# Kernel tuning notes

Measured on AMD Instinct MI355X. Metric: run time of the kernel, lower is better.

## Reference

```python
import jax, jax.numpy as jnp
import numpy as np

D_MODEL = 1024
N_HEAD = 16
DEPTH = D_MODEL // N_HEAD
NEG = -10000.0


def setup_inputs() -> dict:
    key = jax.random.key(0)
    ks = jax.random.split(key, 10)
    B, N = 4, 2048
    s = 1.0 / np.sqrt(D_MODEL)
    inp = {
        "input": jax.random.normal(ks[0], (B, N, D_MODEL), dtype=jnp.float32),
        "mask": jnp.tril(jnp.ones((N, N), dtype=bool)),  # causal; True = attend
        "Wq": jax.random.normal(ks[1], (D_MODEL, D_MODEL), dtype=jnp.float32) * s,
        "bq": jnp.zeros((D_MODEL,), dtype=jnp.float32),
        "Wk": jax.random.normal(ks[2], (D_MODEL, D_MODEL), dtype=jnp.float32) * s,
        "bk": jnp.zeros((D_MODEL,), dtype=jnp.float32),
        "Wv": jax.random.normal(ks[3], (D_MODEL, D_MODEL), dtype=jnp.float32) * s,
        "bv": jnp.zeros((D_MODEL,), dtype=jnp.float32),
        "Wo": jax.random.normal(ks[4], (D_MODEL, D_MODEL), dtype=jnp.float32) * s,
        "bo": jnp.zeros((D_MODEL,), dtype=jnp.float32),
    }
    return inp


def reference(input, mask, Wq, bq, Wk, bk, Wv, bv, Wo, bo):
    b, n, _ = input.shape
    # torch Linear: x @ W.T + b  (dropout is identity in eval)
    q = (input @ Wq.T + bq).reshape(b, n, N_HEAD, DEPTH)
    k = (input @ Wk.T + bk).reshape(b, n, N_HEAD, DEPTH)
    v = (input @ Wv.T + bv).reshape(b, n, N_HEAD, DEPTH)
    # per-head scale is sqrt(depth) (ScaledDotProductAttention built with d_model=depth)
    scale = jnp.sqrt(jnp.asarray(DEPTH, dtype=input.dtype))
    scores = jnp.einsum("bnhd,bmhd->bhnm", q, k) / scale
    scores = jnp.where(mask, scores, NEG)
    attn = jax.nn.softmax(scores, axis=-1)
    out = jnp.einsum("bhnm,bmhd->bnhd", attn, v).reshape(b, n, D_MODEL)
    return out @ Wo.T + bo
```

## Files before the change

kernel.cpp:

```cpp
#include <hip/hip_runtime.h>
#include <hip/hip_bf16.h>
#include <stdint.h>

#define D_MODEL 1024
#define N_HEAD  16
#define DEPTH   64
#define BATCH   4
#define SEQ     2048
#define ROWS    (BATCH*SEQ)
#define LOG2E   1.4426950408889634f
#define QSCALE  0.18033688292839513f

typedef unsigned short u16;
typedef __attribute__((ext_vector_type(8))) short short8;
typedef __attribute__((ext_vector_type(4))) float f32x4;

__device__ inline u16 f2bf(float f) {
  union { float f; unsigned u; } v; v.f = f;
  unsigned r = v.u + 0x7FFFu + ((v.u >> 16) & 1u);
  return (u16)(r >> 16);
}

__device__ inline unsigned cvt_pk_bf16(float lo, float hi) {
  unsigned w;
  asm("v_cvt_pk_bf16_f32 %0, %1, %2" : "=v"(w) : "v"(lo), "v"(hi));
  return w;
}

__device__ inline void gll16(const void* g, void* l) {
  __builtin_amdgcn_global_load_lds(
      (const __attribute__((address_space(1))) void*)g,
      (__attribute__((address_space(3))) void*)l, 16, 0, 0);
}

__global__ __launch_bounds__(256) void cvt_all(
    const float4* __restrict__ X,  const float4* __restrict__ Wq,
    const float4* __restrict__ Wk, const float4* __restrict__ Wv,
    const float4* __restrict__ Wo,
    u16* __restrict__ Xb, u16* __restrict__ Wqkvb, u16* __restrict__ Wob)
{
  const int b = blockIdx.x;
  const float4* src; u16* dst; int lb;
  if      (b < 8192)  { src = X;  dst = Xb;                        lb = b; }
  else if (b < 9216)  { src = Wq; dst = Wqkvb;                     lb = b - 8192; }
  else if (b < 10240) { src = Wk; dst = Wqkvb + D_MODEL*D_MODEL;   lb = b - 9216; }
  else if (b < 11264) { src = Wv; dst = Wqkvb + 2*D_MODEL*D_MODEL; lb = b - 10240; }
  else                { src = Wo; dst = Wob;                       lb = b - 11264; }
  const int i = lb*256 + threadIdx.x;
  float4 v = src[i];
  ushort4 o;
  o.x = f2bf(v.x); o.y = f2bf(v.y); o.z = f2bf(v.z); o.w = f2bf(v.w);
  *(ushort4*)(dst + 4*(size_t)i) = o;
}

__global__ __launch_bounds__(256) void gemm_qkv(
    const u16* __restrict__ A, const u16* __restrict__ Bm,
    const float* __restrict__ bq, const float* __restrict__ bk,
    const float* __restrict__ bvp,
    u16* __restrict__ Qo, u16* __restrict__ Ko, u16* __restrict__ Vo)
{
  constexpr int K = D_MODEL, BK = 64;
  __shared__ __align__(16) u16 As[128*BK];
  __shared__ __align__(16) u16 Bs[128*BK];
  const int tid = threadIdx.x;
  const int wave = tid >> 6, lane = tid & 63;
  const int g = lane >> 4, c = lane & 15;
  const int m0 = blockIdx.x * 128, n0 = blockIdx.y * 128;
  const int wr = (wave >> 1) * 64, wc = (wave & 1) * 64;
  f32x4 acc[4][4] = {};

  int aRow[4], aCol[4];
#pragma unroll
  for (int cc = 0; cc < 4; ++cc) {
    int L = (wave*4 + cc)*1024 + lane*16;
    int U = L ^ (((L >> 7) & 7) << 4);
    aRow[cc] = U >> 7;
    aCol[cc] = (U & 127) >> 1;
  }

  for (int k0 = 0; k0 < K; k0 += BK) {
#pragma unroll
    for (int cc = 0; cc < 4; ++cc) {
      int chunk = wave*4 + cc;
      gll16(A  + (size_t)(m0 + aRow[cc])*K + k0 + aCol[cc], (char*)As + chunk*1024);
      gll16(Bm + (size_t)(n0 + aRow[cc])*K + k0 + aCol[cc], (char*)Bs + chunk*1024);
    }
    __syncthreads();
#pragma unroll
    for (int ks = 0; ks < 2; ++ks) {
      short8 af[4], bf[4];
#pragma unroll
      for (int rb = 0; rb < 4; ++rb) {
        int row = wr + rb*16 + c;
        int addr = (row*128 + ks*64 + g*16) ^ ((row & 7) << 4);
        af[rb] = *(const short8*)((const char*)As + addr);
      }
#pragma unroll
      for (int cb = 0; cb < 4; ++cb) {
        int row = wc + cb*16 + c;
        int addr = (row*128 + ks*64 + g*16) ^ ((row & 7) << 4);
        bf[cb] = *(const short8*)((const char*)Bs + addr);
      }
#pragma unroll
      for (int rb = 0; rb < 4; ++rb)
#pragma unroll
        for (int cb = 0; cb < 4; ++cb)
          acc[rb][cb] = __builtin_amdgcn_mfma_f32_16x16x32_bf16(af[rb], bf[cb], acc[rb][cb], 0, 0, 0);
    }
    __syncthreads();
  }

  const int mode = n0 >> 10;
  const float* bias = (mode == 0) ? bq : (mode == 1) ? bk : bvp;

#pragma unroll
  for (int rb = 0; rb < 4; ++rb) {
#pragma unroll
    for (int cb = 0; cb < 4; ++cb) {
      int colg = n0 + wc + cb*16 + c;
      int cl = colg & 1023;
      int h = cl >> 6, d = cl & 63;
      float bv = bias[cl];
      if (mode == 2) {
        int rg = m0 + wr + rb*16 + g*4;
        int b = rg >> 11, n = rg & 2047;
        ushort4 o;
        o.x = f2bf(acc[rb][cb][0] + bv);
        o.y = f2bf(acc[rb][cb][1] + bv);
        o.z = f2bf(acc[rb][cb][2] + bv);
        o.w = f2bf(acc[rb][cb][3] + bv);
        *(ushort4*)&Vo[(((size_t)(b*N_HEAD + h))*DEPTH + d)*SEQ + n] = o;
      } else {
        u16* dst = (mode == 0) ? Qo : Ko;
        float sc = (mode == 0) ? QSCALE : 1.0f;
#pragma unroll
        for (int r = 0; r < 4; ++r) {
          int rowg = m0 + wr + rb*16 + g*4 + r;
          int b = rowg >> 11, n = rowg & 2047;
          dst[(((size_t)(b*N_HEAD + h))*SEQ + n)*DEPTH + d] = f2bf((acc[rb][cb][r] + bv) * sc);
        }
      }
    }
  }
}

__global__ __launch_bounds__(256) void gemm_out(
    const u16* __restrict__ A, const u16* __restrict__ Bm,
    const float* __restrict__ bias, float* __restrict__ Cout,
    int M, int N, int K)
{
  constexpr int BK = 64;
  __shared__ __align__(16) u16 As[128*BK];
  __shared__ __align__(16) u16 Bs[128*BK];
  const int tid = threadIdx.x;
  const int wave = tid >> 6, lane = tid & 63;
  const int g = lane >> 4, c = lane & 15;
  const int m0 = blockIdx.x * 128, n0 = blockIdx.y * 128;
  const int wr = (wave >> 1) * 64, wc = (wave & 1) * 64;
  f32x4 acc[4][4] = {};

  int aRow[4], aCol[4];
#pragma unroll
  for (int cc = 0; cc < 4; ++cc) {
    int L = (wave*4 + cc)*1024 + lane*16;
    int U = L ^ (((L >> 7) & 7) << 4);
    aRow[cc] = U >> 7;
    aCol[cc] = (U & 127) >> 1;
  }

  for (int k0 = 0; k0 < K; k0 += BK) {
#pragma unroll
    for (int cc = 0; cc < 4; ++cc) {
      int chunk = wave*4 + cc;
      gll16(A  + (size_t)(m0 + aRow[cc])*K + k0 + aCol[cc], (char*)As + chunk*1024);
      gll16(Bm + (size_t)(n0 + aRow[cc])*K + k0 + aCol[cc], (char*)Bs + chunk*1024);
    }
    __syncthreads();
#pragma unroll
    for (int ks = 0; ks < 2; ++ks) {
      short8 af[4], bf[4];
#pragma unroll
      for (int rb = 0; rb < 4; ++rb) {
        int row = wr + rb*16 + c;
        int addr = (row*128 + ks*64 + g*16) ^ ((row & 7) << 4);
        af[rb] = *(const short8*)((const char*)As + addr);
      }
#pragma unroll
      for (int cb = 0; cb < 4; ++cb) {
        int row = wc + cb*16 + c;
        int addr = (row*128 + ks*64 + g*16) ^ ((row & 7) << 4);
        bf[cb] = *(const short8*)((const char*)Bs + addr);
      }
#pragma unroll
      for (int rb = 0; rb < 4; ++rb)
#pragma unroll
        for (int cb = 0; cb < 4; ++cb)
          acc[rb][cb] = __builtin_amdgcn_mfma_f32_16x16x32_bf16(af[rb], bf[cb], acc[rb][cb], 0, 0, 0);
    }
    __syncthreads();
  }

#pragma unroll
  for (int rb = 0; rb < 4; ++rb) {
#pragma unroll
    for (int cb = 0; cb < 4; ++cb) {
      int colg = n0 + wc + cb*16 + c;
      float bv = bias[colg];
#pragma unroll
      for (int r = 0; r < 4; ++r) {
        int rowg = m0 + wr + rb*16 + g*4 + r;
        Cout[(size_t)rowg * N + colg] = acc[rb][cb][r] + bv;
      }
    }
  }
}

__global__ __launch_bounds__(256) void flash(
    const u16* __restrict__ Q, const u16* __restrict__ K,
    const u16* __restrict__ VT, u16* __restrict__ O)
{
  __shared__ __align__(16) u16 Ks[2][64*64];
  __shared__ __align__(16) u16 Vs[2][64*64];
  const int tid = threadIdx.x, wave = tid >> 6, lane = tid & 63;
  const int g = lane >> 4, c = lane & 15;
  const int bid = blockIdx.x;
  const int qt = 31 - (bid >> 6);
  const int bh = bid & 63, b = bh >> 4, h = bh & 15;
  const int q0 = qt * 64;
  const int qg = q0 + wave*16 + c;
  const u16* Qh = Q  + (size_t)bh * SEQ * DEPTH;
  const u16* Kh = K  + (size_t)bh * SEQ * DEPTH;
  const u16* Vh = VT + (size_t)bh * DEPTH * SEQ;

  short8 qf[2];
#pragma unroll
  for (int ks = 0; ks < 2; ++ks)
    qf[ks] = *(const short8*)(Qh + (size_t)qg*DEPTH + ks*32 + g*8);

  f32x4 o[4] = {};
  float m_r = -3.0e38f, l_r = 0.0f;

  const int src1 = (c + (((2*g)  & 3) << 4)) << 2;
  const int src2 = (c + (((2*g+1)& 3) << 4)) << 2;
  const bool hi = (g >> 1) & 1;

  int sRow[2], sCol[2];
#pragma unroll
  for (int cc = 0; cc < 2; ++cc) {
    int L = (wave*2 + cc)*1024 + lane*16;
    int U = L ^ (((L >> 7) & 7) << 4);
    sRow[cc] = U >> 7; sCol[cc] = (U & 127) >> 1;
  }

  auto stage = [&](int t, int bsel) {
    const int kv0 = t * 64;
#pragma unroll
    for (int cc = 0; cc < 2; ++cc) {
      int chunk = wave*2 + cc;
      gll16(Kh + (size_t)(kv0 + sRow[cc])*DEPTH + sCol[cc], (char*)Ks[bsel] + chunk*1024);
      gll16(Vh + (size_t)sRow[cc]*SEQ + kv0 + sCol[cc],     (char*)Vs[bsel] + chunk*1024);
    }
  };

  const int ntiles = qt + 1;
  stage(0, 0);
  __syncthreads();
  int cur = 0;

  for (int t = 0; t < ntiles; ++t) {
    if (t + 1 < ntiles) stage(t + 1, cur ^ 1);
    const int kv0 = t * 64;
    const char* Kc = (const char*)Ks[cur];
    const char* Vc = (const char*)Vs[cur];

    f32x4 s[4] = {};
    __builtin_amdgcn_s_setprio(1);
#pragma unroll
    for (int ks = 0; ks < 2; ++ks)
#pragma unroll
      for (int cb = 0; cb < 4; ++cb) {
        int row = cb*16 + c;
        int addr = (row*128 + ks*64 + g*16) ^ ((row & 7) << 4);
        short8 kf = *(const short8*)(Kc + addr);
        s[cb] = __builtin_amdgcn_mfma_f32_16x16x32_bf16(kf, qf[ks], s[cb], 0, 0, 0);
      }
    __builtin_amdgcn_s_setprio(0);

    if (t == ntiles - 1) {
#pragma unroll
      for (int cb = 0; cb < 4; ++cb)
#pragma unroll
        for (int r = 0; r < 4; ++r)
          if (kv0 + cb*16 + g*4 + r > qg) s[cb][r] = -3.0e38f;
    }

    float pmax = fmaxf(
        fmaxf(fmaxf(fmaxf(s[0][0], s[0][1]), s[0][2]),
              fmaxf(fmaxf(s[0][3], s[1][0]), s[1][1])),
        fmaxf(fmaxf(fmaxf(s[1][2], s[1][3]), s[2][0]),
              fmaxf(fmaxf(s[2][1], s[2][2]), s[2][3])));
    pmax = fmaxf(pmax, fmaxf(fmaxf(s[3][0], s[3][1]), fmaxf(s[3][2], s[3][3])));

    if (__any(pmax > m_r + 8.0f)) {
      float mx = fmaxf(pmax, __shfl_xor(pmax, 16));
      mx = fmaxf(mx, __shfl_xor(mx, 32));
      float mn = fmaxf(m_r, mx);
      float alpha = exp2f(m_r - mn);
      m_r = mn;
      l_r *= alpha;
#pragma unroll
      for (int db = 0; db < 4; ++db)
#pragma unroll
        for (int r = 0; r < 4; ++r) o[db][r] *= alpha;
    }

    float sum = 0.f;
    unsigned pk01[4], pk23[4];
#pragma unroll
    for (int cb = 0; cb < 4; ++cb) {
      float p0 = exp2f(s[cb][0] - m_r);
      float p1 = exp2f(s[cb][1] - m_r);
      float p2 = exp2f(s[cb][2] - m_r);
      float p3 = exp2f(s[cb][3] - m_r);
      sum += (p0 + p1) + (p2 + p3);
      pk01[cb] = cvt_pk_bf16(p0, p1);
      pk23[cb] = cvt_pk_bf16(p2, p3);
    }
    l_r += sum;

#pragma unroll
    for (int js = 0; js < 2; ++js) {
      unsigned a0  = __builtin_amdgcn_ds_bpermute(src1, pk01[2*js]);
      unsigned a0b = __builtin_amdgcn_ds_bpermute(src1, pk01[2*js+1]);
      unsigned a1  = __builtin_amdgcn_ds_bpermute(src1, pk23[2*js]);
      unsigned a1b = __builtin_amdgcn_ds_bpermute(src1, pk23[2*js+1]);
      unsigned b0  = __builtin_amdgcn_ds_bpermute(src2, pk01[2*js]);
      unsigned b0b = __builtin_amdgcn_ds_bpermute(src2, pk01[2*js+1]);
      unsigned b1  = __builtin_amdgcn_ds_bpermute(src2, pk23[2*js]);
      unsigned b1b = __builtin_amdgcn_ds_bpermute(src2, pk23[2*js+1]);
      union { unsigned u[4]; short8 v8; } pf;
      pf.u[0] = hi ? a0b : a0;
      pf.u[1] = hi ? a1b : a1;
      pf.u[2] = hi ? b0b : b0;
      pf.u[3] = hi ? b1b : b1;
      __builtin_amdgcn_s_setprio(1);
#pragma unroll
      for (int db = 0; db < 4; ++db) {
        int row = db*16 + c;
        int addr = (row*128 + js*64 + g*16) ^ ((row & 7) << 4);
        short8 vf = *(const short8*)(Vc + addr);
        o[db] = __builtin_amdgcn_mfma_f32_16x16x32_bf16(vf, pf.v8, o[db], 0, 0, 0);
      }
      __builtin_amdgcn_s_setprio(0);
    }
    __syncthreads();
    cur ^= 1;
  }

  l_r += __shfl_xor(l_r, 16);
  l_r += __shfl_xor(l_r, 32);
  float inv = 1.0f / l_r;
  size_t base = ((size_t)(b*SEQ + qg))*D_MODEL + h*DEPTH;
#pragma unroll
  for (int db = 0; db < 4; ++db) {
    ushort4 w;
    w.x = f2bf(o[db][0] * inv);
    w.y = f2bf(o[db][1] * inv);
    w.z = f2bf(o[db][2] * inv);
    w.w = f2bf(o[db][3] * inv);
    *(ushort4*)&O[base + db*16 + g*4] = w;
  }
}

extern "C" void kernel_launch(void* const* d_in, const int* in_sizes, int n_in,
                              void* d_out, int out_size, void* d_ws, size_t ws_size,
                              hipStream_t stream) {
  const float* X  = (const float*)d_in[0];
  const float* Wq = (const float*)d_in[2];
  const float* bq = (const float*)d_in[3];
  const float* Wk = (const float*)d_in[4];
  const float* bk = (const float*)d_in[5];
  const float* Wv = (const float*)d_in[6];
  const float* bv = (const float*)d_in[7];
  const float* Wo = (const float*)d_in[8];
  const float* bo = (const float*)d_in[9];

  char* w = (char*)d_ws;
  const size_t MB = 1u << 20;
  u16* Xb   = (u16*)(w);
  u16* Qb   = (u16*)(w + 16*MB);
  u16* Kb   = (u16*)(w + 32*MB);
  u16* VTb  = (u16*)(w + 48*MB);
  u16* Ob   = (u16*)(w + 64*MB);
  u16* Wqkv = (u16*)(w + 80*MB);
  u16* Wob  = (u16*)(w + 86*MB);

  cvt_all<<<12288, 256, 0, stream>>>(
      (const float4*)X, (const float4*)Wq, (const float4*)Wk,
      (const float4*)Wv, (const float4*)Wo, Xb, Wqkv, Wob);

  gemm_qkv<<<dim3(ROWS/128, 3*D_MODEL/128), 256, 0, stream>>>(
      Xb, Wqkv, bq, bk, bv, Qb, Kb, VTb);

  flash<<<2048, 256, 0, stream>>>(Qb, Kb, VTb, Ob);

  gemm_out<<<dim3(ROWS/128, D_MODEL/128), 256, 0, stream>>>(
      Ob, Wob, bo, (float*)d_out, ROWS, D_MODEL, D_MODEL);
}
```

Measured before the change: 287.3 us.

## Retile QKV GEMM to 256x256 with 512 threads and double-buffered LDS prefetch

Rewrites the fused QKV projection GEMM to use 256x256 output tiles per 512-thread block, with each wave computing 128x64. It double-buffers the LDS tiles, issuing async global-to-LDS loads two k-steps ahead and gating them with explicit vmcnt waits and barriers. MFMA bursts run at raised wave priority. The aim is to hide global load latency and raise arithmetic intensity per LDS byte, at the cost of 128 KB LDS per block (one block per CU), more accumulator registers, and fewer blocks (384) in the grid.

```diff
diff --git a/kernel.cpp b/kernel.cpp
--- a/kernel.cpp
+++ b/kernel.cpp
@@ -53,91 +53,132 @@
   *(ushort4*)(dst + 4*(size_t)i) = o;
 }
 
-__global__ __launch_bounds__(256) void gemm_qkv(
+__global__ __launch_bounds__(512) void gemm_qkv(
     const u16* __restrict__ A, const u16* __restrict__ Bm,
     const float* __restrict__ bq, const float* __restrict__ bk,
     const float* __restrict__ bvp,
     u16* __restrict__ Qo, u16* __restrict__ Ko, u16* __restrict__ Vo)
 {
-  constexpr int K = D_MODEL, BK = 64;
-  __shared__ __align__(16) u16 As[128*BK];
-  __shared__ __align__(16) u16 Bs[128*BK];
+  constexpr int K = D_MODEL;
+  constexpr int NT = 16;
+  __shared__ __align__(16) u16 As[2][256*64];
+  __shared__ __align__(16) u16 Bs[2][256*64];
   const int tid = threadIdx.x;
   const int wave = tid >> 6, lane = tid & 63;
   const int g = lane >> 4, c = lane & 15;
-  const int m0 = blockIdx.x * 128, n0 = blockIdx.y * 128;
-  const int wr = (wave >> 1) * 64, wc = (wave & 1) * 64;
-  f32x4 acc[4][4] = {};
-
-  int aRow[4], aCol[4];
-#pragma unroll
-  for (int cc = 0; cc < 4; ++cc) {
-    int L = (wave*4 + cc)*1024 + lane*16;
+  const int wm = wave >> 2, wn = wave & 3;
+  const int m0 = blockIdx.x * 256, n0 = blockIdx.y * 256;
+  f32x4 acc[8][4] = {};
+
+  int sRow[4], sCol[4];
+#pragma unroll
+  for (int s = 0; s < 4; ++s) {
+    int L = s*8192 + tid*16;
     int U = L ^ (((L >> 7) & 7) << 4);
-    aRow[cc] = U >> 7;
-    aCol[cc] = (U & 127) >> 1;
-  }
-
-  for (int k0 = 0; k0 < K; k0 += BK) {
-#pragma unroll
-    for (int cc = 0; cc < 4; ++cc) {
-      int chunk = wave*4 + cc;
-      gll16(A  + (size_t)(m0 + aRow[cc])*K + k0 + aCol[cc], (char*)As + chunk*1024);
-      gll16(Bm + (size_t)(n0 + aRow[cc])*K + k0 + aCol[cc], (char*)Bs + chunk*1024);
-    }
-    __syncthreads();
-#pragma unroll
-    for (int ks = 0; ks < 2; ++ks) {
-      short8 af[4], bf[4];
-#pragma unroll
-      for (int rb = 0; rb < 4; ++rb) {
-        int row = wr + rb*16 + c;
-        int addr = (row*128 + ks*64 + g*16) ^ ((row & 7) << 4);
-        af[rb] = *(const short8*)((const char*)As + addr);
-      }
-#pragma unroll
-      for (int cb = 0; cb < 4; ++cb) {
-        int row = wc + cb*16 + c;
-        int addr = (row*128 + ks*64 + g*16) ^ ((row & 7) << 4);
-        bf[cb] = *(const short8*)((const char*)Bs + addr);
-      }
-#pragma unroll
-      for (int rb = 0; rb < 4; ++rb)
-#pragma unroll
-        for (int cb = 0; cb < 4; ++cb)
-          acc[rb][cb] = __builtin_amdgcn_mfma_f32_16x16x32_bf16(af[rb], bf[cb], acc[rb][cb], 0, 0, 0);
-    }
-    __syncthreads();
+    sRow[s] = U >> 7;
+    sCol[s] = (U & 127) >> 1;
+  }
+
+  auto stage = [&](int kt, int bsel) {
+#pragma unroll
+    for (int s = 0; s < 4; ++s)
+      gll16(A  + (size_t)(m0 + sRow[s])*K + kt*64 + sCol[s],
+            (char*)As[bsel] + s*8192 + tid*16);
+#pragma unroll
+    for (int s = 0; s < 4; ++s)
+      gll16(Bm + (size_t)(n0 + sRow[s])*K + kt*64 + sCol[s],
+            (char*)Bs[bsel] + s*8192 + tid*16);
+  };
+
+  stage(0, 0);
+  stage(1, 1);
+  asm volatile("s_waitcnt vmcnt(8)" ::: "memory");
+  __builtin_amdgcn_sched_barrier(0);
+  __builtin_amdgcn_s_barrier();
+  __builtin_amdgcn_sched_barrier(0);
+
+  for (int k = 0; k < NT; ++k) {
+    const int cur = k & 1;
+    const char* Ac = (const char*)As[cur];
+    const char* Bc = (const char*)Bs[cur];
+
+#pragma unroll
+    for (int p = 0; p < 4; ++p) {
+      const int mh = p >> 1, nh = p & 1;
+      short8 af[4][2], bf[2][2];
+#pragma unroll
+      for (int ii = 0; ii < 4; ++ii) {
+        int row = wm*128 + (mh*4 + ii)*16 + c;
+#pragma unroll
+        for (int ks = 0; ks < 2; ++ks) {
+          int addr = (row*128 + ks*64 + g*16) ^ ((row & 7) << 4);
+          af[ii][ks] = *(const short8*)(Ac + addr);
+        }
+      }
+#pragma unroll
+      for (int jj = 0; jj < 2; ++jj) {
+        int row = wn*64 + (nh*2 + jj)*16 + c;
+#pragma unroll
+        for (int ks = 0; ks < 2; ++ks) {
+          int addr = (row*128 + ks*64 + g*16) ^ ((row & 7) << 4);
+          bf[jj][ks] = *(const short8*)(Bc + addr);
+        }
+      }
+      __builtin_amdgcn_sched_barrier(0);
+      __builtin_amdgcn_s_barrier();
+      __builtin_amdgcn_sched_barrier(0);
+      __builtin_amdgcn_s_setprio(1);
+#pragma unroll
+      for (int ks = 0; ks < 2; ++ks)
+#pragma unroll
+        for (int ii = 0; ii < 4; ++ii)
+#pragma unroll
+          for (int jj = 0; jj < 2; ++jj)
+            acc[mh*4 + ii][nh*2 + jj] = __builtin_amdgcn_mfma_f32_16x16x32_bf16(
+                af[ii][ks], bf[jj][ks], acc[mh*4 + ii][nh*2 + jj], 0, 0, 0);
+      __builtin_amdgcn_s_setprio(0);
+    }
+
+    __builtin_amdgcn_sched_barrier(0);
+    __builtin_amdgcn_s_barrier();
+    __builtin_amdgcn_sched_barrier(0);
+    if (k + 2 < NT) stage(k + 2, cur);
+    if (k + 1 < NT) {
+      if (k + 2 < NT) asm volatile("s_waitcnt vmcnt(8)" ::: "memory");
+      else            asm volatile("s_waitcnt vmcnt(0)" ::: "memory");
+      __builtin_amdgcn_sched_barrier(0);
+      __builtin_amdgcn_s_barrier();
+      __builtin_amdgcn_sched_barrier(0);
+    }
   }
 
   const int mode = n0 >> 10;
   const float* bias = (mode == 0) ? bq : (mode == 1) ? bk : bvp;
-
-#pragma unroll
-  for (int rb = 0; rb < 4; ++rb) {
-#pragma unroll
-    for (int cb = 0; cb < 4; ++cb) {
-      int colg = n0 + wc + cb*16 + c;
+#pragma unroll
+  for (int i = 0; i < 8; ++i) {
+#pragma unroll
+    for (int j = 0; j < 4; ++j) {
+      int colg = n0 + wn*64 + j*16 + c;
       int cl = colg & 1023;
       int h = cl >> 6, d = cl & 63;
       float bv = bias[cl];
       if (mode == 2) {
-        int rg = m0 + wr + rb*16 + g*4;
+        int rg = m0 + wm*128 + i*16 + g*4;
         int b = rg >> 11, n = rg & 2047;
         ushort4 o;
-        o.x = f2bf(acc[rb][cb][0] + bv);
-        o.y = f2bf(acc[rb][cb][1] + bv);
-        o.z = f2bf(acc[rb][cb][2] + bv);
-        o.w = f2bf(acc[rb][cb][3] + bv);
+        o.x = f2bf(acc[i][j][0] + bv);
+        o.y = f2bf(acc[i][j][1] + bv);
+        o.z = f2bf(acc[i][j][2] + bv);
+        o.w = f2bf(acc[i][j][3] + bv);
         *(ushort4*)&Vo[(((size_t)(b*N_HEAD + h))*DEPTH + d)*SEQ + n] = o;
       } else {
         u16* dst = (mode == 0) ? Qo : Ko;
         float sc = (mode == 0) ? QSCALE : 1.0f;
 #pragma unroll
         for (int r = 0; r < 4; ++r) {
-          int rowg = m0 + wr + rb*16 + g*4 + r;
+          int rowg = m0 + wm*128 + i*16 + g*4 + r;
           int b = rowg >> 11, n = rowg & 2047;
-          dst[(((size_t)(b*N_HEAD + h))*SEQ + n)*DEPTH + d] = f2bf((acc[rb][cb][r] + bv) * sc);
+          dst[(((size_t)(b*N_HEAD + h))*SEQ + n)*DEPTH + d] = f2bf((acc[i][j][r] + bv) * sc);
         }
       }
     }
@@ -399,7 +440,7 @@
       (const float4*)X, (const float4*)Wq, (const float4*)Wk,
       (const float4*)Wv, (const float4*)Wo, Xb, Wqkv, Wob);
 
-  gemm_qkv<<<dim3(ROWS/128, 3*D_MODEL/128), 256, 0, stream>>>(
+  gemm_qkv<<<dim3(ROWS/256, 3*D_MODEL/256), 512, 0, stream>>>(
       Xb, Wqkv, bq, bk, bv, Qb, Kb, VTb);
 
   flash<<<2048, 256, 0, stream>>>(Qb, Kb, VTb, Ob);
```

Measured after the change: 304.6 us. +6.0%, slower.
